# Kernel tuning notes

Measured on AMD Instinct MI355X. Metric: run time of the kernel, lower is better.

## Reference

```python
import jax, jax.numpy as jnp
import numpy as np

B, C, H, W = 16, 64, 64, 64
HW = H * W            # = dim = 4096
R = 4                 # reduction_ratio
NH = 8                # head_num
EPS = 1e-5


def setup_inputs() -> dict:
    key = jax.random.key(0)
    ks = jax.random.split(key, 8)
    s = 0.02  # weight init scale
    return {
        "x": jax.random.normal(ks[0], (B, C, H, W), jnp.float32),
        "ln1_w": jnp.ones((C,), jnp.float32),
        "ln1_b": jnp.zeros((C,), jnp.float32),
        "ln2_w": jnp.ones((C,), jnp.float32),
        "ln2_b": jnp.zeros((C,), jnp.float32),
        "W_rk": jax.random.normal(ks[1], (C * R, C), jnp.float32) * s,
        "W_rv": jax.random.normal(ks[2], (C * R, C), jnp.float32) * s,
        "W_q": jax.random.normal(ks[3], (HW, HW), jnp.float32) * s,
        "W_k": jax.random.normal(ks[4], (HW // R, HW // R), jnp.float32) * s,
        "W_v": jax.random.normal(ks[5], (HW // R, HW // R), jnp.float32) * s,
        "W_o": jax.random.normal(ks[6], (HW, HW), jnp.float32) * s,
    }


def _ln(x, w, b):
    # LayerNorm over last axis
    mu = jnp.mean(x, axis=-1, keepdims=True)
    var = jnp.mean((x - mu) ** 2, axis=-1, keepdims=True)
    return (x - mu) / jnp.sqrt(var + EPS) * w + b


def reference(x, ln1_w, ln1_b, ln2_w, ln2_b, W_rk, W_rv, W_q, W_k, W_v, W_o):
    b, c, h, w = x.shape
    hw = h * w
    # ln1: LayerNorm2d == per-pixel LayerNorm over channels
    xn = _ln(x.transpose(0, 2, 3, 1), ln1_w, ln1_b)      # [B,H,W,C]
    xf = xn.reshape(b, hw, c)                            # [B,HW,C] (row-major HW)
    # K/V spatial reduction: 'a (cd r) b -> a cd (b r)'
    kv = xf.reshape(b, hw // R, R, c).transpose(0, 1, 3, 2).reshape(b, hw // R, c * R)
    k = _ln(kv @ W_rk, ln2_w, ln2_b)                     # [B,HW/R,C]
    v = _ln(kv @ W_rv, ln2_w, ln2_b)                     # [B,HW/R,C]
    # projections over the SPATIAL axis (dim = HW)
    q = xf.transpose(0, 2, 1) @ W_q                      # [B,C,HW]
    k = k.transpose(0, 2, 1) @ W_k                       # [B,C,HW/R]
    v = v.transpose(0, 2, 1) @ W_v                       # [B,C,HW/R]
    Lq = hw // NH
    Lk = (hw // R) // NH
    # split heads along spatial axis, attend over channel dim C
    qh = q.reshape(b, c, NH, Lq).transpose(0, 2, 3, 1)   # [B,h,Lq,C]
    kh = k.reshape(b, c, NH, Lk).transpose(0, 2, 3, 1)   # [B,h,Lk,C]
    vh = v.reshape(b, c, NH, Lk).transpose(0, 2, 3, 1)   # [B,h,Lk,C]
    scale = float(hw // NH) ** 0.5
    attn = jax.nn.softmax(jnp.einsum('bhqc,bhkc->bhqk', qh, kh) / scale, axis=-1)
    # dropout is identity at inference
    o = jnp.einsum('bhqk,bhkc->bhqc', attn, vh)          # [B,h,Lq,C]
    # concat_head: heads become outer blocks of the spatial axis
    o = o.transpose(0, 3, 1, 2).reshape(b, c, hw)        # [B,C,HW]
    o = o @ W_o                                          # [B,C,HW]
    return o.reshape(b, c, h, w) + x
```

## Files before the change

### kernel.cpp

```cpp
#include <hip/hip_runtime.h>

typedef unsigned short u16;
typedef unsigned int u32;
typedef __attribute__((ext_vector_type(8))) __bf16 bf16x8;
typedef __attribute__((ext_vector_type(4))) float f32x4;
typedef __attribute__((ext_vector_type(4))) unsigned int u32x4;

#define MFMA16(a, b, c) __builtin_amdgcn_mfma_f32_16x16x32_bf16((a), (b), (c), 0, 0, 0)

__device__ __forceinline__ u16 f2bf(float f) {
  unsigned u = __float_as_uint(f);
  u += 0x7FFFu + ((u >> 16) & 1u);
  return (u16)(u >> 16);
}

typedef __attribute__((address_space(1))) const unsigned char gU8;
typedef __attribute__((address_space(3))) unsigned char sU8;
__device__ __forceinline__ void gload16(const void* g, void* l) {
  __builtin_amdgcn_global_load_lds((gU8*)g, (sU8*)l, 16, 0, 0);
}

__device__ __forceinline__ void wt_body(const float* __restrict__ W, u16* __restrict__ Wt,
                                        int K, int N, int bid, float* tile) {
  int ntn = N >> 6;
  int kt = bid / ntn, nt = bid % ntn;
  int t = threadIdx.x;
  const float* src = W + (size_t)kt * 64 * N + (size_t)nt * 64;
#pragma unroll
  for (int i = 0; i < 4; ++i) {
    int idx = t + i * 256, row = idx >> 4, c4 = idx & 15;
    f32x4 v = *(const f32x4*)&src[(size_t)row * N + c4 * 4];
#pragma unroll
    for (int j = 0; j < 4; ++j) tile[row * 65 + c4 * 4 + j] = v[j];
  }
  __syncthreads();
  u16* dst = Wt + (size_t)nt * 64 * K + (size_t)kt * 64;
#pragma unroll
  for (int i = 0; i < 2; ++i) {
    int idx = t + i * 256, nn = idx >> 3, k8 = idx & 7;
    u16 o[8];
#pragma unroll
    for (int j = 0; j < 8; ++j) o[j] = f2bf(tile[(k8 * 8 + j) * 65 + nn]);
    u32x4 pk;
#pragma unroll
    for (int j = 0; j < 4; ++j) pk[j] = (u32)o[2 * j] | ((u32)o[2 * j + 1] << 16);
    *(u32x4*)&dst[(size_t)nn * K + k8 * 8] = pk;
  }
}

__device__ __forceinline__ void wperm_body(const float* __restrict__ Wrk, const float* __restrict__ Wrv,
                                           u16* __restrict__ Wtk, u16* __restrict__ Wtv, int bid) {
  int idx = bid * 256 + threadIdx.x;
  int cp = idx >> 8, f = idx & 255;
  int k = ((f & 63) << 2) | (f >> 6);
  Wtk[idx] = f2bf(Wrk[k * 64 + cp]);
  Wtv[idx] = f2bf(Wrv[k * 64 + cp]);
}

__device__ __forceinline__ void ln1_body(const float* __restrict__ x, const float* __restrict__ w,
                                         const float* __restrict__ bias, u16* __restrict__ xf_pc,
                                         u16* __restrict__ xfT, int bid, float* tile) {
  int b = bid >> 6, p0 = (bid & 63) << 6;
  int t = threadIdx.x;
  const float* xb = x + (size_t)b * 64 * 4096;
#pragma unroll
  for (int i = 0; i < 4; ++i) {
    int idx = t + i * 256, c = idx >> 4, p4 = idx & 15;
    f32x4 v = *(const f32x4*)&xb[(size_t)c * 4096 + p0 + p4 * 4];
#pragma unroll
    for (int j = 0; j < 4; ++j) tile[c * 65 + p4 * 4 + j] = v[j];
  }
  __syncthreads();
  int lane = t & 63, wv = t >> 6;
  float gw = w[lane], gb = bias[lane];
  for (int pi = 0; pi < 16; ++pi) {
    int p = wv * 16 + pi;
    float v = tile[lane * 65 + p];
    float s = v, s2 = v * v;
#pragma unroll
    for (int m = 1; m < 64; m <<= 1) { s += __shfl_xor(s, m); s2 += __shfl_xor(s2, m); }
    float mean = s * (1.0f / 64.0f);
    float var = s2 * (1.0f / 64.0f) - mean * mean;
    float y = (v - mean) * rsqrtf(var + 1e-5f) * gw + gb;
    tile[lane * 65 + p] = y;
  }
  __syncthreads();
  u16* xfb = xf_pc + (size_t)b * 4096 * 64;
  u16* xtb = xfT + (size_t)b * 64 * 4096;
#pragma unroll
  for (int i = 0; i < 2; ++i) {
    int idx = t + i * 256, p = idx >> 3, c8 = idx & 7;
    u16 o[8];
#pragma unroll
    for (int j = 0; j < 8; ++j) o[j] = f2bf(tile[(c8 * 8 + j) * 65 + p]);
    u32x4 pk;
#pragma unroll
    for (int j = 0; j < 4; ++j) pk[j] = (u32)o[2 * j] | ((u32)o[2 * j + 1] << 16);
    *(u32x4*)&xfb[(size_t)(p0 + p) * 64 + c8 * 8] = pk;
  }
#pragma unroll
  for (int i = 0; i < 2; ++i) {
    int idx = t + i * 256, c = idx >> 3, p8 = idx & 7;
    u16 o[8];
#pragma unroll
    for (int j = 0; j < 8; ++j) o[j] = f2bf(tile[c * 65 + p8 * 8 + j]);
    u32x4 pk;
#pragma unroll
    for (int j = 0; j < 4; ++j) pk[j] = (u32)o[2 * j] | ((u32)o[2 * j + 1] << 16);
    *(u32x4*)&xtb[(size_t)c * 4096 + p0 + p8 * 8] = pk;
  }
}

__global__ __launch_bounds__(256) void prep_kernel(
    const float* __restrict__ W_q, u16* __restrict__ Wt_q,
    const float* __restrict__ W_o, u16* __restrict__ Wt_o,
    const float* __restrict__ W_k, u16* __restrict__ Wt_k,
    const float* __restrict__ W_v, u16* __restrict__ Wt_v,
    const float* __restrict__ W_rk, const float* __restrict__ W_rv,
    u16* __restrict__ Wt_rk, u16* __restrict__ Wt_rv,
    const float* __restrict__ x, const float* __restrict__ ln1w, const float* __restrict__ ln1b,
    u16* __restrict__ xf_pc, u16* __restrict__ xfT) {
  __shared__ float tile[64 * 65];
  int bid = blockIdx.x;
  if (bid < 4096)       wt_body(W_q, Wt_q, 4096, 4096, bid, tile);
  else if (bid < 8192)  wt_body(W_o, Wt_o, 4096, 4096, bid - 4096, tile);
  else if (bid < 8448)  wt_body(W_k, Wt_k, 1024, 1024, bid - 8192, tile);
  else if (bid < 8704)  wt_body(W_v, Wt_v, 1024, 1024, bid - 8448, tile);
  else if (bid < 8768)  wperm_body(W_rk, W_rv, Wt_rk, Wt_rv, bid - 8704);
  else                  ln1_body(x, ln1w, ln1b, xf_pc, xfT, bid - 8768, tile);
}

__global__ __launch_bounds__(256) void kv_kernel(const u16* __restrict__ xf_pc,
                                                 const u16* __restrict__ Wtk, const u16* __restrict__ Wtv,
                                                 const float* __restrict__ ln2w, const float* __restrict__ ln2b,
                                                 u16* __restrict__ kT, u16* __restrict__ vT) {
  __shared__ __align__(16) u16 As[64 * 264];
  __shared__ __align__(16) u16 Bk[64 * 264];
  __shared__ __align__(16) u16 Bv[64 * 264];
  u16* Tk = As;
  u16* Tv = As + 64 * 72;
  int b = blockIdx.x >> 4, s0 = (blockIdx.x & 15) << 6;
  int t = threadIdx.x;
  const u16* Asrc = xf_pc + (size_t)b * 4096 * 64 + (size_t)s0 * 256;
#pragma unroll
  for (int i = 0; i < 8; ++i) {
    int id = t + i * 256, row = id >> 5, c16 = id & 31;
    *(u32x4*)&As[row * 264 + c16 * 8] = *(const u32x4*)&Asrc[(size_t)row * 256 + c16 * 8];
    *(u32x4*)&Bk[row * 264 + c16 * 8] = *(const u32x4*)&Wtk[(size_t)row * 256 + c16 * 8];
    *(u32x4*)&Bv[row * 264 + c16 * 8] = *(const u32x4*)&Wtv[(size_t)row * 256 + c16 * 8];
  }
  __syncthreads();
  int lane = t & 63, wv = t >> 6, lo = lane & 15, hi = lane >> 4;
  f32x4 acck[4] = {}, accv[4] = {};
  int arow = (wv * 16 + lo) * 264 + hi * 8;
#pragma unroll
  for (int kk = 0; kk < 8; ++kk) {
    bf16x8 a = *(const bf16x8*)&As[arow + kk * 32];
#pragma unroll
    for (int nf = 0; nf < 4; ++nf) {
      bf16x8 bk = *(const bf16x8*)&Bk[(nf * 16 + lo) * 264 + kk * 32 + hi * 8];
      bf16x8 bv = *(const bf16x8*)&Bv[(nf * 16 + lo) * 264 + kk * 32 + hi * 8];
      acck[nf] = MFMA16(a, bk, acck[nf]);
      accv[nf] = MFMA16(a, bv, accv[nf]);
    }
  }
  __syncthreads();
  float w2[4], b2[4];
#pragma unroll
  for (int nf = 0; nf < 4; ++nf) { w2[nf] = ln2w[nf * 16 + lo]; b2[nf] = ln2b[nf * 16 + lo]; }
#pragma unroll
  for (int r = 0; r < 4; ++r) {
    float sk = 0.f, sk2 = 0.f, sv = 0.f, sv2 = 0.f;
#pragma unroll
    for (int nf = 0; nf < 4; ++nf) {
      float a = acck[nf][r], c = accv[nf][r];
      sk += a; sk2 += a * a; sv += c; sv2 += c * c;
    }
#pragma unroll
    for (int m = 1; m < 16; m <<= 1) {
      sk += __shfl_xor(sk, m); sk2 += __shfl_xor(sk2, m);
      sv += __shfl_xor(sv, m); sv2 += __shfl_xor(sv2, m);
    }
    float mk = sk * (1.f / 64.f), vk = sk2 * (1.f / 64.f) - mk * mk, rk = rsqrtf(vk + 1e-5f);
    float mv = sv * (1.f / 64.f), vv = sv2 * (1.f / 64.f) - mv * mv, rv = rsqrtf(vv + 1e-5f);
    int srow = wv * 16 + hi * 4 + r;
#pragma unroll
    for (int nf = 0; nf < 4; ++nf) {
      Tk[(nf * 16 + lo) * 72 + srow] = f2bf((acck[nf][r] - mk) * rk * w2[nf] + b2[nf]);
      Tv[(nf * 16 + lo) * 72 + srow] = f2bf((accv[nf][r] - mv) * rv * w2[nf] + b2[nf]);
    }
  }
  __syncthreads();
  u16* kdst = kT + (size_t)b * 64 * 1024 + s0;
  u16* vdst = vT + (size_t)b * 64 * 1024 + s0;
#pragma unroll
  for (int i = 0; i < 16; ++i) {
    int idx = t + i * 256, cp = idx >> 6, s = idx & 63;
    kdst[(size_t)cp * 1024 + s] = Tk[cp * 72 + s];
    vdst[(size_t)cp * 1024 + s] = Tv[cp * 72 + s];
  }
}

__device__ __forceinline__ void stage_tile(const u16* Ab, const u16* Bb, int K, int kt,
                                           u16* As, u16* Bs, int wv, int lane) {
  int gr = lane >> 3;
  int gcol = (lane & 7) * 8;
  const u16* a0 = Ab + (size_t)kt * 64 + gcol;
  const u16* b0 = Bb + (size_t)kt * 64 + gcol;
#pragma unroll
  for (int i = 0; i < 4; ++i) {
    int chunk = wv * 4 + i;
    int row = chunk * 8 + gr;
    gload16(a0 + (size_t)row * K, As + chunk * 512);
    gload16(b0 + (size_t)row * K, Bs + chunk * 512);
  }
}

__device__ __forceinline__ void compute_tile(const u16* As, const u16* Bs, f32x4 acc[4][4],
                                             int wm, int wn, int lo, int hi) {
#pragma unroll
  for (int kk = 0; kk < 2; ++kk) {
    bf16x8 a[4], bb[4];
#pragma unroll
    for (int i = 0; i < 4; ++i) {
      a[i]  = *(const bf16x8*)&As[(wm + i * 16 + lo) * 64 + kk * 32 + hi * 8];
      bb[i] = *(const bf16x8*)&Bs[(wn + i * 16 + lo) * 64 + kk * 32 + hi * 8];
    }
#pragma unroll
    for (int mi = 0; mi < 4; ++mi)
#pragma unroll
      for (int ni = 0; ni < 4; ++ni)
        acc[mi][ni] = MFMA16(a[mi], bb[ni], acc[mi][ni]);
  }
}

template <int EPI>
__device__ void gemm_body(const u16* __restrict__ A, const u16* __restrict__ Bm,
                          u16* __restrict__ Cc, int N, int K, int chunkStride,
                          int mt, int nt, int koff, int nk, u16* lds) {
  int t = threadIdx.x, lane = t & 63, wv = t >> 6;
  int wm = (wv >> 1) * 64, wn = (wv & 1) * 64;
  int lo = lane & 15, hi = lane >> 4;
  f32x4 acc[4][4] = {};
  const u16* Ab = A + (size_t)mt * 128 * K + koff;
  const u16* Bb = Bm + (size_t)nt * 128 * K + koff;
  u16* As = lds;
  u16* Bs = lds + 8192;
  for (int kt = 0; kt < nk; ++kt) {
    stage_tile(Ab, Bb, K, kt, As, Bs, wv, lane);
    __syncthreads();
    compute_tile(As, Bs, acc, wm, wn, lo, hi);
    __syncthreads();
  }
#pragma unroll
  for (int mi = 0; mi < 4; ++mi)
#pragma unroll
    for (int ni = 0; ni < 4; ++ni)
#pragma unroll
      for (int r = 0; r < 4; ++r) {
        int m = mt * 128 + wm + mi * 16 + hi * 4 + r;
        int n = nt * 128 + wn + ni * 16 + lo;
        float v = acc[mi][ni][r];
        if constexpr (EPI == 0) {
          Cc[(size_t)m * N + n] = f2bf(v);
        } else {
          Cc[(size_t)(n >> 6) * chunkStride + (size_t)m * 64 + (n & 63)] = f2bf(v);
        }
      }
}

__global__ __launch_bounds__(256, 3) void qkv_kernel(
    const u16* __restrict__ Wt_q, const u16* __restrict__ xfT, u16* __restrict__ q_t,
    const u16* __restrict__ Wt_k, const u16* __restrict__ k_lnT, u16* __restrict__ kproj,
    const u16* __restrict__ v_lnT, const u16* __restrict__ Wt_v, u16* __restrict__ vproj) {
  __shared__ __align__(16) u16 lds[16384];
  int bid = blockIdx.x;
  if (bid < 1024) {
    int log = (bid & 7) * 128 + (bid >> 3);
    int kh = log >> 8, tile = log & 255, mt = tile >> 3, nt = tile & 7;
    gemm_body<1>(Wt_q, xfT, q_t + (size_t)kh * 4194304, 1024, 4096, 4096 * 64,
                 mt, nt, kh * 1024, 16, lds);
  } else if (bid < 1088) {
    int id = bid - 1024;
    gemm_body<1>(Wt_k, k_lnT, kproj, 1024, 1024, 1024 * 64, id >> 3, id & 7, 0, 16, lds);
  } else {
    int id = bid - 1088;
    gemm_body<0>(v_lnT, Wt_v, vproj, 1024, 1024, 0, id >> 3, id & 7, 0, 16, lds);
  }
}

__global__ __launch_bounds__(256, 3) void ogemm_kernel(const u16* __restrict__ o2,
                                                       const u16* __restrict__ Wt_o,
                                                       u16* __restrict__ o_part) {
  __shared__ __align__(16) u16 lds[16384];
  int bid = blockIdx.x;
  int log = (bid & 7) * 64 + (bid >> 3);
  int kh = log >> 8, tile = log & 255, mt = tile >> 5, nt = tile & 31;
  gemm_body<0>(o2, Wt_o, o_part + (size_t)kh * 4194304, 4096, 4096, 0,
               mt, nt, kh * 2048, 32, lds);
}

__global__ __launch_bounds__(256) void oreduce_kernel(const float* __restrict__ x,
                                                      const u16* __restrict__ p0,
                                                      const u16* __restrict__ p1,
                                                      float* __restrict__ out) {
  size_t base = ((size_t)blockIdx.x * 256 + threadIdx.x) * 8;
  u32x4 a = *(const u32x4*)&p0[base];
  u32x4 b = *(const u32x4*)&p1[base];
  f32x4 x0 = *(const f32x4*)&x[base];
  f32x4 x1 = *(const f32x4*)&x[base + 4];
  float r[8];
#pragma unroll
  for (int j = 0; j < 4; ++j) {
    r[2 * j]     = __uint_as_float(a[j] << 16) + __uint_as_float(b[j] << 16);
    r[2 * j + 1] = __uint_as_float(a[j] & 0xFFFF0000u) + __uint_as_float(b[j] & 0xFFFF0000u);
  }
  f32x4 o0, o1;
#pragma unroll
  for (int j = 0; j < 4; ++j) { o0[j] = r[j] + x0[j]; o1[j] = r[4 + j] + x1[j]; }
  *(f32x4*)&out[base] = o0;
  *(f32x4*)&out[base + 4] = o1;
}

__global__ __launch_bounds__(256) void attn_kernel(const u16* __restrict__ qp, const u16* __restrict__ kp,
                                                   const u16* __restrict__ vp, u16* __restrict__ o2) {
  __shared__ __align__(16) u16 Qs[128 * 72];
  __shared__ __align__(16) u16 Ks[128 * 72];
  __shared__ __align__(16) u16 Vs[64 * 136];
  __shared__ __align__(16) u16 Ps[128 * 136];
  int qt = blockIdx.x & 3, h = (blockIdx.x >> 2) & 7, b = blockIdx.x >> 5;
  int t = threadIdx.x, lane = t & 63, wv = t >> 6;
  int lo = lane & 15, hi = lane >> 4;
  const u16* qsrc = qp + (size_t)b * 262144 + (size_t)(h * 512 + qt * 128) * 64;
  const u16* ksrc = kp + (size_t)b * 1024 * 64 + (size_t)(h * 128) * 64;
  const u16* vsrc = vp + (size_t)b * 64 * 1024 + h * 128;
#pragma unroll
  for (int i = 0; i < 4; ++i) {
    int id = t + i * 256, row = id >> 3, c8 = id & 7;
    size_t goff = (size_t)row * 64 + c8 * 8;
    float f[8] = {0.f, 0.f, 0.f, 0.f, 0.f, 0.f, 0.f, 0.f};
#pragma unroll
    for (int kh = 0; kh < 4; ++kh) {
      u32x4 pk = *(const u32x4*)&qsrc[(size_t)kh * 4194304 + goff];
#pragma unroll
      for (int j = 0; j < 4; ++j) {
        f[2 * j]     += __uint_as_float(pk[j] << 16);
        f[2 * j + 1] += __uint_as_float(pk[j] & 0xFFFF0000u);
      }
    }
    u32x4 pko;
#pragma unroll
    for (int j = 0; j < 4; ++j) pko[j] = (u32)f2bf(f[2 * j]) | ((u32)f2bf(f[2 * j + 1]) << 16);
    *(u32x4*)&Qs[row * 72 + c8 * 8] = pko;
  }
#pragma unroll
  for (int i = 0; i < 4; ++i) {
    int id = t + i * 256;
    int row = id >> 3, c16 = id & 7;
    *(u32x4*)&Ks[row * 72 + c16 * 8] = *(const u32x4*)&ksrc[(size_t)row * 64 + c16 * 8];
    int vrow = id >> 4, v16 = id & 15;
    *(u32x4*)&Vs[vrow * 136 + v16 * 8] = *(const u32x4*)&vsrc[(size_t)vrow * 1024 + v16 * 8];
  }
  __syncthreads();
  f32x4 s[2][8] = {};
#pragma unroll
  for (int kk = 0; kk < 2; ++kk) {
    bf16x8 a0 = *(const bf16x8*)&Qs[(wv * 32 + lo) * 72 + kk * 32 + hi * 8];
    bf16x8 a1 = *(const bf16x8*)&Qs[(wv * 32 + 16 + lo) * 72 + kk * 32 + hi * 8];
#pragma unroll
    for (int ni = 0; ni < 8; ++ni) {
      bf16x8 bb = *(const bf16x8*)&Ks[(ni * 16 + lo) * 72 + kk * 32 + hi * 8];
      s[0][ni] = MFMA16(a0, bb, s[0][ni]);
      s[1][ni] = MFMA16(a1, bb, s[1][ni]);
    }
  }
  const float inv_scale = 0.044194173824159216f;
#pragma unroll
  for (int mi = 0; mi < 2; ++mi)
#pragma unroll
    for (int ni = 0; ni < 8; ++ni) s[mi][ni] *= inv_scale;
#pragma unroll
  for (int mi = 0; mi < 2; ++mi) {
#pragma unroll
    for (int r = 0; r < 4; ++r) {
      float mx = -1e30f;
#pragma unroll
      for (int ni = 0; ni < 8; ++ni) mx = fmaxf(mx, s[mi][ni][r]);
#pragma unroll
      for (int m = 1; m < 16; m <<= 1) mx = fmaxf(mx, __shfl_xor(mx, m));
      float p[8], sum = 0.f;
#pragma unroll
      for (int ni = 0; ni < 8; ++ni) { p[ni] = __expf(s[mi][ni][r] - mx); sum += p[ni]; }
#pragma unroll
      for (int m = 1; m < 16; m <<= 1) sum += __shfl_xor(sum, m);
      float rs = 1.0f / sum;
      int row = wv * 32 + mi * 16 + hi * 4 + r;
#pragma unroll
      for (int ni = 0; ni < 8; ++ni) Ps[row * 136 + ni * 16 + lo] = f2bf(p[ni] * rs);
    }
  }
  __syncthreads();
  f32x4 o[4][2] = {};
#pragma unroll
  for (int kk = 0; kk < 4; ++kk) {
    bf16x8 b0 = *(const bf16x8*)&Ps[(wv * 32 + lo) * 136 + kk * 32 + hi * 8];
    bf16x8 b1 = *(const bf16x8*)&Ps[(wv * 32 + 16 + lo) * 136 + kk * 32 + hi * 8];
#pragma unroll
    for (int mi = 0; mi < 4; ++mi) {
      bf16x8 a = *(const bf16x8*)&Vs[(mi * 16 + lo) * 136 + kk * 32 + hi * 8];
      o[mi][0] = MFMA16(a, b0, o[mi][0]);
      o[mi][1] = MFMA16(a, b1, o[mi][1]);
    }
  }
  u16* od = o2 + (size_t)b * 64 * 4096 + h * 512 + qt * 128;
#pragma unroll
  for (int mi = 0; mi < 4; ++mi)
#pragma unroll
    for (int ni = 0; ni < 2; ++ni)
#pragma unroll
      for (int r = 0; r < 4; ++r) {
        int c = mi * 16 + hi * 4 + r;
        int lq = wv * 32 + ni * 16 + lo;
        od[(size_t)c * 4096 + lq] = f2bf(o[mi][ni][r]);
      }
}

extern "C" void kernel_launch(void* const* d_in, const int* in_sizes, int n_in,
                              void* d_out, int out_size, void* d_ws, size_t ws_size,
                              hipStream_t stream) {
  (void)in_sizes; (void)n_in; (void)out_size; (void)ws_size;
  const float* x    = (const float*)d_in[0];
  const float* ln1w = (const float*)d_in[1];
  const float* ln1b = (const float*)d_in[2];
  const float* ln2w = (const float*)d_in[3];
  const float* ln2b = (const float*)d_in[4];
  const float* W_rk = (const float*)d_in[5];
  const float* W_rv = (const float*)d_in[6];
  const float* W_q  = (const float*)d_in[7];
  const float* W_k  = (const float*)d_in[8];
  const float* W_v  = (const float*)d_in[9];
  const float* W_o  = (const float*)d_in[10];

  char* ws = (char*)d_ws;
  size_t off = 0;
  auto alloc = [&](size_t bytes) { char* p = ws + off; off += bytes; return p; };
  u16* Wt_q  = (u16*)alloc(4096ull * 4096 * 2);
  u16* Wt_o  = (u16*)alloc(4096ull * 4096 * 2);
  u16* Wt_k  = (u16*)alloc(1024ull * 1024 * 2);
  u16* Wt_v  = (u16*)alloc(1024ull * 1024 * 2);
  u16* Wt_rk = (u16*)alloc(64ull * 256 * 2);
  u16* Wt_rv = (u16*)alloc(64ull * 256 * 2);
  u16* xf_pc = (u16*)alloc(16ull * 4096 * 64 * 2);
  u16* xfT   = (u16*)alloc(16ull * 64 * 4096 * 2);
  u16* k_lnT = (u16*)alloc(16ull * 64 * 1024 * 2);
  u16* v_lnT = (u16*)alloc(16ull * 64 * 1024 * 2);
  u16* q_t   = (u16*)alloc(4ull * 16 * 4096 * 64 * 2);
  u16* kproj = (u16*)alloc(16ull * 1024 * 64 * 2);
  u16* vproj = (u16*)alloc(16ull * 64 * 1024 * 2);
  u16* o2     = xfT;
  u16* o_part = Wt_q;

  prep_kernel<<<9792, 256, 0, stream>>>(W_q, Wt_q, W_o, Wt_o, W_k, Wt_k, W_v, Wt_v,
                                        W_rk, W_rv, Wt_rk, Wt_rv, x, ln1w, ln1b, xf_pc, xfT);
  kv_kernel<<<256, 256, 0, stream>>>(xf_pc, Wt_rk, Wt_rv, ln2w, ln2b, k_lnT, v_lnT);
  qkv_kernel<<<1152, 256, 0, stream>>>(Wt_q, xfT, q_t, Wt_k, k_lnT, kproj, v_lnT, Wt_v, vproj);
  attn_kernel<<<512, 256, 0, stream>>>(q_t, kproj, vproj, o2);
  ogemm_kernel<<<512, 256, 0, stream>>>(o2, Wt_o, o_part);
  oreduce_kernel<<<2048, 256, 0, stream>>>(x, o_part, o_part + 4194304, (float*)d_out);
}
```

Before: 209.0 us.

## Triple-buffer GEMM LDS with async prefetch, XOR swizzle, and batched prep loads

```diff
diff --git a/kernel.cpp b/kernel.cpp
--- a/kernel.cpp
+++ b/kernel.cpp
@@ -26,25 +26,33 @@
   int kt = bid / ntn, nt = bid % ntn;
   int t = threadIdx.x;
   const float* src = W + (size_t)kt * 64 * N + (size_t)nt * 64;
+  f32x4 r[4];
 #pragma unroll
   for (int i = 0; i < 4; ++i) {
     int idx = t + i * 256, row = idx >> 4, c4 = idx & 15;
-    f32x4 v = *(const f32x4*)&src[(size_t)row * N + c4 * 4];
-#pragma unroll
-    for (int j = 0; j < 4; ++j) tile[row * 65 + c4 * 4 + j] = v[j];
-  }
-  __syncthreads();
+    r[i] = *(const f32x4*)&src[(size_t)row * N + c4 * 4];
+  }
+#pragma unroll
+  for (int i = 0; i < 4; ++i) {
+    int idx = t + i * 256, row = idx >> 4, c4 = idx & 15;
+#pragma unroll
+    for (int j = 0; j < 4; ++j) tile[row * 65 + c4 * 4 + j] = r[i][j];
+  }
+  __syncthreads();
+  int nn0 = t >> 3, k8 = t & 7;
+  float v[2][8];
+#pragma unroll
+  for (int i = 0; i < 2; ++i)
+#pragma unroll
+    for (int j = 0; j < 8; ++j) v[i][j] = tile[(k8 * 8 + j) * 65 + nn0 + i * 32];
   u16* dst = Wt + (size_t)nt * 64 * K + (size_t)kt * 64;
 #pragma unroll
   for (int i = 0; i < 2; ++i) {
-    int idx = t + i * 256, nn = idx >> 3, k8 = idx & 7;
-    u16 o[8];
-#pragma unroll
-    for (int j = 0; j < 8; ++j) o[j] = f2bf(tile[(k8 * 8 + j) * 65 + nn]);
     u32x4 pk;
 #pragma unroll
-    for (int j = 0; j < 4; ++j) pk[j] = (u32)o[2 * j] | ((u32)o[2 * j + 1] << 16);
-    *(u32x4*)&dst[(size_t)nn * K + k8 * 8] = pk;
+    for (int j = 0; j < 4; ++j)
+      pk[j] = (u32)f2bf(v[i][2 * j]) | ((u32)f2bf(v[i][2 * j + 1]) << 16);
+    *(u32x4*)&dst[(size_t)(nn0 + i * 32) * K + k8 * 8] = pk;
   }
 }
 
@@ -63,51 +71,65 @@
   int b = bid >> 6, p0 = (bid & 63) << 6;
   int t = threadIdx.x;
   const float* xb = x + (size_t)b * 64 * 4096;
+  f32x4 r[4];
 #pragma unroll
   for (int i = 0; i < 4; ++i) {
     int idx = t + i * 256, c = idx >> 4, p4 = idx & 15;
-    f32x4 v = *(const f32x4*)&xb[(size_t)c * 4096 + p0 + p4 * 4];
-#pragma unroll
-    for (int j = 0; j < 4; ++j) tile[c * 65 + p4 * 4 + j] = v[j];
-  }
-  __syncthreads();
-  int lane = t & 63, wv = t >> 6;
+    r[i] = *(const f32x4*)&xb[(size_t)c * 4096 + p0 + p4 * 4];
+  }
+#pragma unroll
+  for (int i = 0; i < 4; ++i) {
+    int idx = t + i * 256, c = idx >> 4, p4 = idx & 15;
+#pragma unroll
+    for (int j = 0; j < 4; ++j) tile[c * 65 + p4 * 4 + j] = r[i][j];
+  }
+  __syncthreads();
+  int lane = t & 63, wvx = t >> 6;
   float gw = w[lane], gb = bias[lane];
-  for (int pi = 0; pi < 16; ++pi) {
-    int p = wv * 16 + pi;
-    float v = tile[lane * 65 + p];
-    float s = v, s2 = v * v;
-#pragma unroll
-    for (int m = 1; m < 64; m <<= 1) { s += __shfl_xor(s, m); s2 += __shfl_xor(s2, m); }
-    float mean = s * (1.0f / 64.0f);
-    float var = s2 * (1.0f / 64.0f) - mean * mean;
-    float y = (v - mean) * rsqrtf(var + 1e-5f) * gw + gb;
-    tile[lane * 65 + p] = y;
+#pragma unroll
+  for (int pp = 0; pp < 16; pp += 2) {
+    int p = wvx * 16 + pp;
+    float v0 = tile[lane * 65 + p], v1 = tile[lane * 65 + p + 1];
+    float s0 = v0, q0 = v0 * v0, s1 = v1, q1 = v1 * v1;
+#pragma unroll
+    for (int m = 1; m < 64; m <<= 1) {
+      s0 += __shfl_xor(s0, m); q0 += __shfl_xor(q0, m);
+      s1 += __shfl_xor(s1, m); q1 += __shfl_xor(q1, m);
+    }
+    float mu0 = s0 * (1.0f / 64.0f), var0 = q0 * (1.0f / 64.0f) - mu0 * mu0;
+    float mu1 = s1 * (1.0f / 64.0f), var1 = q1 * (1.0f / 64.0f) - mu1 * mu1;
+    tile[lane * 65 + p]     = (v0 - mu0) * rsqrtf(var0 + 1e-5f) * gw + gb;
+    tile[lane * 65 + p + 1] = (v1 - mu1) * rsqrtf(var1 + 1e-5f) * gw + gb;
   }
   __syncthreads();
   u16* xfb = xf_pc + (size_t)b * 4096 * 64;
   u16* xtb = xfT + (size_t)b * 64 * 4096;
+  int i0 = t >> 3, j8 = t & 7;
+  float vc[2][8];
+#pragma unroll
+  for (int i = 0; i < 2; ++i)
+#pragma unroll
+    for (int j = 0; j < 8; ++j) vc[i][j] = tile[(j8 * 8 + j) * 65 + i0 + i * 32];
 #pragma unroll
   for (int i = 0; i < 2; ++i) {
-    int idx = t + i * 256, p = idx >> 3, c8 = idx & 7;
-    u16 o[8];
-#pragma unroll
-    for (int j = 0; j < 8; ++j) o[j] = f2bf(tile[(c8 * 8 + j) * 65 + p]);
     u32x4 pk;
 #pragma unroll
-    for (int j = 0; j < 4; ++j) pk[j] = (u32)o[2 * j] | ((u32)o[2 * j + 1] << 16);
-    *(u32x4*)&xfb[(size_t)(p0 + p) * 64 + c8 * 8] = pk;
-  }
+    for (int j = 0; j < 4; ++j)
+      pk[j] = (u32)f2bf(vc[i][2 * j]) | ((u32)f2bf(vc[i][2 * j + 1]) << 16);
+    *(u32x4*)&xfb[(size_t)(p0 + i0 + i * 32) * 64 + j8 * 8] = pk;
+  }
+  float vr[2][8];
+#pragma unroll
+  for (int i = 0; i < 2; ++i)
+#pragma unroll
+    for (int j = 0; j < 8; ++j) vr[i][j] = tile[(i0 + i * 32) * 65 + j8 * 8 + j];
 #pragma unroll
   for (int i = 0; i < 2; ++i) {
-    int idx = t + i * 256, c = idx >> 3, p8 = idx & 7;
-    u16 o[8];
-#pragma unroll
-    for (int j = 0; j < 8; ++j) o[j] = f2bf(tile[c * 65 + p8 * 8 + j]);
     u32x4 pk;
 #pragma unroll
-    for (int j = 0; j < 4; ++j) pk[j] = (u32)o[2 * j] | ((u32)o[2 * j + 1] << 16);
-    *(u32x4*)&xtb[(size_t)c * 4096 + p0 + p8 * 8] = pk;
+    for (int j = 0; j < 4; ++j)
+      pk[j] = (u32)f2bf(vr[i][2 * j]) | ((u32)f2bf(vr[i][2 * j + 1]) << 16);
+    *(u32x4*)&xtb[(size_t)(i0 + i * 32) * 4096 + p0 + j8 * 8] = pk;
   }
 }
 
@@ -203,14 +225,14 @@
 
 __device__ __forceinline__ void stage_tile(const u16* Ab, const u16* Bb, int K, int kt,
                                            u16* As, u16* Bs, int wv, int lane) {
-  int gr = lane >> 3;
-  int gcol = (lane & 7) * 8;
+  int r8 = lane >> 3;
+  int gcol = ((lane & 7) ^ r8) << 3;
   const u16* a0 = Ab + (size_t)kt * 64 + gcol;
   const u16* b0 = Bb + (size_t)kt * 64 + gcol;
 #pragma unroll
   for (int i = 0; i < 4; ++i) {
     int chunk = wv * 4 + i;
-    int row = chunk * 8 + gr;
+    int row = chunk * 8 + r8;
     gload16(a0 + (size_t)row * K, As + chunk * 512);
     gload16(b0 + (size_t)row * K, Bs + chunk * 512);
   }
@@ -218,13 +240,15 @@
 
 __device__ __forceinline__ void compute_tile(const u16* As, const u16* Bs, f32x4 acc[4][4],
                                              int wm, int wn, int lo, int hi) {
+  int sa = lo & 7;
 #pragma unroll
   for (int kk = 0; kk < 2; ++kk) {
+    int slot = ((kk * 4 + hi) ^ sa) << 3;
     bf16x8 a[4], bb[4];
 #pragma unroll
     for (int i = 0; i < 4; ++i) {
-      a[i]  = *(const bf16x8*)&As[(wm + i * 16 + lo) * 64 + kk * 32 + hi * 8];
-      bb[i] = *(const bf16x8*)&Bs[(wn + i * 16 + lo) * 64 + kk * 32 + hi * 8];
+      a[i]  = *(const bf16x8*)&As[(wm + i * 16 + lo) * 64 + slot];
+      bb[i] = *(const bf16x8*)&Bs[(wn + i * 16 + lo) * 64 + slot];
     }
 #pragma unroll
     for (int mi = 0; mi < 4; ++mi)
@@ -244,13 +268,21 @@
   f32x4 acc[4][4] = {};
   const u16* Ab = A + (size_t)mt * 128 * K + koff;
   const u16* Bb = Bm + (size_t)nt * 128 * K + koff;
-  u16* As = lds;
-  u16* Bs = lds + 8192;
+  u16* buf[3] = {lds, lds + 16384, lds + 32768};
+  stage_tile(Ab, Bb, K, 0, buf[0], buf[0] + 8192, wv, lane);
+  stage_tile(Ab, Bb, K, 1, buf[1], buf[1] + 8192, wv, lane);
   for (int kt = 0; kt < nk; ++kt) {
-    stage_tile(Ab, Bb, K, kt, As, Bs, wv, lane);
-    __syncthreads();
-    compute_tile(As, Bs, acc, wm, wn, lo, hi);
-    __syncthreads();
+    if (kt + 1 < nk) asm volatile("s_waitcnt vmcnt(8)" ::: "memory");
+    else             asm volatile("s_waitcnt vmcnt(0)" ::: "memory");
+    __builtin_amdgcn_s_barrier();
+    __builtin_amdgcn_sched_barrier(0);
+    int nxt = kt + 2;
+    if (nxt < nk) {
+      u16* nb = buf[nxt % 3];
+      stage_tile(Ab, Bb, K, nxt, nb, nb + 8192, wv, lane);
+    }
+    u16* cb = buf[kt % 3];
+    compute_tile(cb, cb + 8192, acc, wm, wn, lo, hi);
   }
 #pragma unroll
   for (int mi = 0; mi < 4; ++mi)
@@ -269,11 +301,11 @@
       }
 }
 
-__global__ __launch_bounds__(256, 3) void qkv_kernel(
+__global__ __launch_bounds__(256, 1) void qkv_kernel(
     const u16* __restrict__ Wt_q, const u16* __restrict__ xfT, u16* __restrict__ q_t,
     const u16* __restrict__ Wt_k, const u16* __restrict__ k_lnT, u16* __restrict__ kproj,
     const u16* __restrict__ v_lnT, const u16* __restrict__ Wt_v, u16* __restrict__ vproj) {
-  __shared__ __align__(16) u16 lds[16384];
+  __shared__ __align__(16) u16 lds[49152];
   int bid = blockIdx.x;
   if (bid < 1024) {
     int log = (bid & 7) * 128 + (bid >> 3);
@@ -289,10 +321,10 @@
   }
 }
 
-__global__ __launch_bounds__(256, 3) void ogemm_kernel(const u16* __restrict__ o2,
+__global__ __launch_bounds__(256, 1) void ogemm_kernel(const u16* __restrict__ o2,
                                                        const u16* __restrict__ Wt_o,
                                                        u16* __restrict__ o_part) {
-  __shared__ __align__(16) u16 lds[16384];
+  __shared__ __align__(16) u16 lds[49152];
   int bid = blockIdx.x;
   int log = (bid & 7) * 64 + (bid >> 3);
   int kh = log >> 8, tile = log & 255, mt = tile >> 5, nt = tile & 31;
```

Result: slower. 244.0 us (+16.8%).
